# Kernel optimization log

Measured on AMD Instinct MI355X. Metric: run time of the kernel, lower is better.

## Reference

```python
import math
import jax, jax.numpy as jnp
import numpy as np

B, T, D, H, E, K = 2, 2048, 1024, 16, 8, 2
HD = D // H                      # head_dim = 64
CAP = math.ceil(1.25 * B * T / E)  # capacity per expert = 640
NEG = -1e9


def setup_inputs() -> dict:
    key = jax.random.key(0)
    ks = jax.random.split(key, 8)
    s = 0.02
    return {
        "x": jax.random.normal(ks[0], (B, T, D), jnp.float32),
        "ln1_g": jnp.ones((D,), jnp.float32),
        "ln1_b": jnp.zeros((D,), jnp.float32),
        "w_qkv": jax.random.normal(ks[1], (3 * D, D), jnp.float32) * s,
        "w_proj": jax.random.normal(ks[2], (D, D), jnp.float32) * s,
        "ln2_g": jnp.ones((D,), jnp.float32),
        "ln2_b": jnp.zeros((D,), jnp.float32),
        "w_gate": jax.random.normal(ks[3], (E, D), jnp.float32) * s,
        "w1": jax.random.normal(ks[4], (E, D, 4 * D), jnp.float32) * s,
        "b1": jnp.zeros((E, 4 * D), jnp.float32),
        "w2": jax.random.normal(ks[5], (E, 4 * D, D), jnp.float32) * s,
        "b2": jnp.zeros((E, D), jnp.float32),
    }


def _layernorm(x, g, b, eps=1e-5):
    m = x.mean(-1, keepdims=True)
    v = ((x - m) ** 2).mean(-1, keepdims=True)
    return (x - m) * jax.lax.rsqrt(v + eps) * g + b


def _rope(q, k):
    # q,k: [B,T,H,HD]; rotate-half RoPE with half_dim = HD//2 frequencies
    half = HD // 2
    pos = jnp.arange(T, dtype=jnp.float32)[:, None]
    inv_freq = 1.0 / (10000.0 ** (jnp.arange(0, HD, 2, dtype=jnp.float32) / HD))
    ang = pos * inv_freq                              # [T, half]
    sin = jnp.sin(ang)[None, :, None, :]
    cos = jnp.cos(ang)[None, :, None, :]

    def rot(t):
        t1, t2 = t[..., :half], t[..., half:]
        return jnp.concatenate([t1 * cos - t2 * sin, t1 * sin + t2 * cos], -1)

    return rot(q), rot(k)


def _attention(x, w_qkv, w_proj):
    qkv = (x @ w_qkv.T).reshape(B, T, H, 3 * HD)
    q, k, v = jnp.split(qkv, 3, axis=-1)              # each [B,T,H,HD]
    q, k = _rope(q, k)
    scores = jnp.einsum('bqhd,bkhd->bhqk', q, k) / math.sqrt(HD)
    causal = jnp.tril(jnp.ones((T, T), bool))
    scores = jnp.where(causal, scores, NEG)
    probs = jax.nn.softmax(scores, axis=-1)
    out = jnp.einsum('bhqk,bkhd->bqhd', probs, v).reshape(B, T, D)
    return out @ w_proj.T


def _sparse_moe(x2d, w_gate, w1, b1, w2, b2):
    # x2d: [N, D] flattened tokens. Eval mode: no noise, no dropout.
    N = x2d.shape[0]
    gates = jax.nn.softmax((x2d @ w_gate.T).astype(jnp.float32), axis=-1)  # [N,E]
    gate_vals, idx = jax.lax.top_k(gates, K)          # [N,K]
    gate_vals = gate_vals.astype(x2d.dtype)

    # Capacity enforcement: token order position within each expert
    mask = jnp.zeros((N, E), bool).at[jnp.arange(N)[:, None], idx].set(True)
    pos = jnp.cumsum(mask.astype(jnp.int32), axis=0) * mask - 1   # [N,E]
    keep = (pos < CAP) & mask
    slot = jnp.take_along_axis(pos, idx, axis=1)      # [N,K]
    kept = jnp.take_along_axis(keep, idx, axis=1)     # [N,K] bool

    # Dispatch: dropped tokens go to pad slot CAP (masked out at combine)
    slot_w = jnp.where(kept, slot, CAP).reshape(-1)   # [N*K]
    e_flat = idx.reshape(-1)                          # [N*K]
    xk = jnp.broadcast_to(x2d[:, None, :], (N, K, D)).reshape(-1, D)
    xk = xk * kept.reshape(-1, 1)
    buf = jnp.zeros((E, CAP + 1, D), x2d.dtype).at[e_flat, slot_w].set(xk)

    # Grouped expert MLP (GELU exact, matching nn.GELU default)
    h = jax.nn.gelu(jnp.einsum('ecd,edf->ecf', buf, w1) + b1[:, None, :],
                    approximate=False)
    out = jnp.einsum('ecf,efd->ecd', h, w2) + b2[:, None, :]

    # Combine: gather each token's expert output, weight by gate, mask drops
    y = out[e_flat, slot_w].reshape(N, K, D) * (gate_vals * kept)[..., None]
    return y.sum(axis=1)


def reference(x, ln1_g, ln1_b, w_qkv, w_proj, ln2_g, ln2_b,
              w_gate, w1, b1, w2, b2):
    h = x + _attention(_layernorm(x, ln1_g, ln1_b), w_qkv, w_proj)
    moe_in = _layernorm(h, ln2_g, ln2_b)
    moe_out = _sparse_moe(moe_in.reshape(B * T, D), w_gate, w1, b1, w2, b2)
    return h + moe_out.reshape(B, T, D)
```

## Files before the change

### kernel.cpp

```cpp
#include <hip/hip_runtime.h>
#include <hip/hip_bf16.h>

typedef __bf16 bf16;
typedef __attribute__((ext_vector_type(8))) __bf16 bf16x8;
typedef __attribute__((ext_vector_type(4))) __bf16 bf16x4;
typedef __attribute__((ext_vector_type(4))) float f32x4;
typedef __attribute__((ext_vector_type(16))) float f32x16;

#define NB 2
#define NT 2048
#define ND 1024
#define NH 16
#define HD_ 64
#define NE 8
#define NCAP 640
#define NTOK 4096
#define NDFF 4096

static __device__ __forceinline__ f32x4 mfma16(bf16x8 a, bf16x8 b, f32x4 c) {
  return __builtin_amdgcn_mfma_f32_16x16x32_bf16(a, b, c, 0, 0, 0);
}
static __device__ __forceinline__ f32x16 mfma32(bf16x8 a, bf16x8 b, f32x16 c) {
  return __builtin_amdgcn_mfma_f32_32x32x16_bf16(a, b, c, 0, 0, 0);
}
static __device__ __forceinline__ unsigned pk2(float a, float b) {
  union { __bf16 h[2]; unsigned u; } z;
  z.h[0] = (__bf16)a; z.h[1] = (__bf16)b;
  return z.u;
}
static __device__ __forceinline__ void gload_lds16(const bf16* g, bf16* l) {
  __builtin_amdgcn_global_load_lds(
      (const __attribute__((address_space(1))) unsigned int*)g,
      (__attribute__((address_space(3))) unsigned int*)l, 16, 0, 0);
}

__global__ __launch_bounds__(256) void cvt_k(const float* __restrict__ in,
                                             bf16* __restrict__ out, int n4) {
  int i = blockIdx.x * 256 + threadIdx.x;
  int stride = gridDim.x * 256;
  for (; i < n4; i += stride) {
    f32x4 v = ((const f32x4*)in)[i];
    bf16x4 o;
    o[0] = (bf16)v[0]; o[1] = (bf16)v[1]; o[2] = (bf16)v[2]; o[3] = (bf16)v[3];
    ((bf16x4*)out)[i] = o;
  }
}

__global__ __launch_bounds__(256) void transpose_k(const float* __restrict__ in,
                                                   bf16* __restrict__ out, int R, int C) {
  __shared__ float tile[64][65];
  const size_t zoff = (size_t)blockIdx.z * R * C;
  in += zoff; out += zoff;
  const int c0 = blockIdx.x * 64, r0 = blockIdx.y * 64;
  const int tx = threadIdx.x & 15, ty = threadIdx.x >> 4;
#pragma unroll
  for (int i = 0; i < 4; i++) {
    const int r = i * 16 + ty;
    f32x4 v = *(const f32x4*)(in + (size_t)(r0 + r) * C + c0 + tx * 4);
    *(f32x4*)&tile[r][tx * 4] = v;
  }
  __syncthreads();
#pragma unroll
  for (int i = 0; i < 4; i++) {
    const int rr = i * 16 + ty;
    bf16x4 o;
#pragma unroll
    for (int j = 0; j < 4; j++) o[j] = (bf16)tile[tx * 4 + j][rr];
    *(bf16x4*)(out + (size_t)(c0 + rr) * R + r0 + tx * 4) = o;
  }
}

__global__ __launch_bounds__(256) void transpose_v_k(const bf16* __restrict__ v,
                                                     bf16* __restrict__ vT) {
  __shared__ bf16 tile[32][33];
  int bh = blockIdx.z;
  const bf16* in = v + (size_t)bh * NT * HD_;
  bf16* out = vT + (size_t)bh * HD_ * NT;
  int t0 = blockIdx.x * 32, d0 = blockIdx.y * 32;
  int tx = threadIdx.x, ty = threadIdx.y;
#pragma unroll
  for (int i = 0; i < 4; i++)
    tile[ty + i * 8][tx] = in[(size_t)(t0 + ty + i * 8) * HD_ + d0 + tx];
  __syncthreads();
#pragma unroll
  for (int i = 0; i < 4; i++)
    out[(size_t)(d0 + ty + i * 8) * NT + t0 + tx] = tile[tx][ty + i * 8];
}

__global__ void rope_tab_k(float* __restrict__ tab) {
  int t = blockIdx.x, i = threadIdx.x;
  float inv = powf(10000.f, -(float)(2 * i) * (1.f / 64.f));
  float ang = (float)t * inv;
  float s, c;
  sincosf(ang, &s, &c);
  tab[(t * 32 + i) * 2] = s;
  tab[(t * 32 + i) * 2 + 1] = c;
}

template <bool BF16OUT>
__global__ __launch_bounds__(256) void ln_k(const float* __restrict__ in,
                                            const float* __restrict__ g,
                                            const float* __restrict__ bb,
                                            bf16* __restrict__ outb,
                                            float* __restrict__ outf) {
  const int row = blockIdx.x;
  const float* xr = in + (size_t)row * ND;
  const int tid = threadIdx.x, lane = tid & 63, wid = tid >> 6;
  f32x4 v = ((const f32x4*)xr)[tid];
  float s = v[0] + v[1] + v[2] + v[3];
  float sq = v[0] * v[0] + v[1] * v[1] + v[2] * v[2] + v[3] * v[3];
#pragma unroll
  for (int m = 1; m < 64; m <<= 1) {
    s += __shfl_xor(s, m, 64);
    sq += __shfl_xor(sq, m, 64);
  }
  __shared__ float red[8];
  if (lane == 0) { red[wid] = s; red[4 + wid] = sq; }
  __syncthreads();
  s = red[0] + red[1] + red[2] + red[3];
  sq = red[4] + red[5] + red[6] + red[7];
  float mean = s * (1.f / 1024.f);
  float var = sq * (1.f / 1024.f) - mean * mean;
  float rs = rsqrtf(var + 1e-5f);
#pragma unroll
  for (int c = 0; c < 4; c++) {
    int col = tid * 4 + c;
    float y = (v[c] - mean) * rs * g[col] + bb[col];
    if constexpr (BF16OUT) outb[(size_t)row * ND + col] = (bf16)y;
    else outf[(size_t)row * ND + col] = y;
  }
}

#define EPI_SPLIT_QKV 0
#define EPI_ADD_X 1
#define EPI_BIAS_GELU 2
#define EPI_STORE 3

template <int EPI, int STAGE, bool PAD>
__global__ __launch_bounds__(256) void gemm_bt_k(
    const bf16* __restrict__ A, const bf16* __restrict__ Bw,
    const int M, const int N, const int K, const int nsplit,
    const size_t zA, const size_t zB, const size_t zOut, const size_t zBias,
    const float* __restrict__ bias, const float* __restrict__ Xadd,
    void* __restrict__ Out, bf16* __restrict__ k_out, bf16* __restrict__ v_out) {
  const int z = blockIdx.z;
  const int ze = z / nsplit;
  const int kc = z - ze * nsplit;
  const int klen = K / nsplit;
  const int kb = kc * klen;
  const int nst = klen / 64;
  const int m0 = blockIdx.y * 128, n0 = blockIdx.x * 128;
  const int tid = threadIdx.x, lane = tid & 63, wid = tid >> 6;
  const int wm = (wid >> 1) * 64, wn = (wid & 1) * 64;
  const int l15 = lane & 15, ksl = lane >> 4;
  constexpr int LDB = (STAGE == 1 && PAD) ? 72 : 64;
  __shared__ __align__(16) bf16 As[128 * LDB];
  __shared__ __align__(16) bf16 Bs[128 * LDB];
  f32x4 acc[4][4];
#pragma unroll
  for (int i = 0; i < 4; i++)
#pragma unroll
    for (int j = 0; j < 4; j++) acc[i][j] = (f32x4){0.f, 0.f, 0.f, 0.f};

  if constexpr (STAGE == 0) {
    const int lr = lane >> 3, lc = (lane & 7) * 8;
    const bf16* Ag = A + zA * ze + (size_t)(m0 + wid * 32 + lr) * K + kb + lc;
    const bf16* Bg = Bw + zB * ze + (size_t)(n0 + wid * 32 + lr) * K + kb + lc;
    for (int s = 0; s < nst; ++s) {
      __syncthreads();
#pragma unroll
      for (int it = 0; it < 4; it++) {
        gload_lds16(Ag + (size_t)(it * 8) * K + s * 64, &As[(wid * 32 + it * 8) * 64]);
        gload_lds16(Bg + (size_t)(it * 8) * K + s * 64, &Bs[(wid * 32 + it * 8) * 64]);
      }
      __syncthreads();
#pragma unroll
      for (int kk = 0; kk < 2; kk++) {
        bf16x8 af[4], bfr[4];
        const int ko = kk * 32 + ksl * 8;
#pragma unroll
        for (int i = 0; i < 4; i++)
          af[i] = *(const bf16x8*)&As[(wm + i * 16 + l15) * 64 + ko];
#pragma unroll
        for (int j = 0; j < 4; j++)
          bfr[j] = *(const bf16x8*)&Bs[(wn + j * 16 + l15) * 64 + ko];
#pragma unroll
        for (int i = 0; i < 4; i++)
#pragma unroll
          for (int j = 0; j < 4; j++)
            acc[i][j] = mfma16(af[i], bfr[j], acc[i][j]);
      }
    }
  } else {
    const int sr = tid >> 3, sc = (tid & 7) * 8;
    const bf16* Ag = A + zA * ze + (size_t)(m0 + sr) * K + kb + sc;
    const bf16* Bg = Bw + zB * ze + (size_t)(n0 + sr) * K + kb + sc;
    bf16x8 av[4], bv[4];
#pragma unroll
    for (int it = 0; it < 4; it++) {
      av[it] = *(const bf16x8*)(Ag + (size_t)(it * 32) * K);
      bv[it] = *(const bf16x8*)(Bg + (size_t)(it * 32) * K);
    }
    for (int s = 0; s < nst; ++s) {
      __syncthreads();
#pragma unroll
      for (int it = 0; it < 4; it++) {
        *(bf16x8*)&As[(sr + it * 32) * LDB + sc] = av[it];
        *(bf16x8*)&Bs[(sr + it * 32) * LDB + sc] = bv[it];
      }
      __syncthreads();
      if (s + 1 < nst) {
#pragma unroll
        for (int it = 0; it < 4; it++) {
          av[it] = *(const bf16x8*)(Ag + (size_t)(it * 32) * K + (s + 1) * 64);
          bv[it] = *(const bf16x8*)(Bg + (size_t)(it * 32) * K + (s + 1) * 64);
        }
      }
#pragma unroll
      for (int kk = 0; kk < 2; kk++) {
        bf16x8 af[4], bfr[4];
        const int ko = kk * 32 + ksl * 8;
#pragma unroll
        for (int i = 0; i < 4; i++)
          af[i] = *(const bf16x8*)&As[(wm + i * 16 + l15) * LDB + ko];
#pragma unroll
        for (int j = 0; j < 4; j++)
          bfr[j] = *(const bf16x8*)&Bs[(wn + j * 16 + l15) * LDB + ko];
#pragma unroll
        for (int i = 0; i < 4; i++)
#pragma unroll
          for (int j = 0; j < 4; j++)
            acc[i][j] = mfma16(af[i], bfr[j], acc[i][j]);
      }
    }
  }

#pragma unroll
  for (int i = 0; i < 4; i++) {
#pragma unroll
    for (int j = 0; j < 4; j++) {
      const int mb = m0 + wm + i * 16 + ksl * 4;
      const int nc = n0 + wn + j * 16 + l15;
#pragma unroll
      for (int r = 0; r < 4; r++) {
        const int mr = mb + r;
        float vacc = acc[i][j][r];
        if constexpr (EPI == EPI_SPLIT_QKV) {
          const int h = nc / 192;
          const int rr = nc - h * 192;
          const int which = rr >> 6;
          const int d = rr & 63;
          const int b = mr >> 11, t = mr & 2047;
          bf16* dst = (which == 0) ? (bf16*)Out : (which == 1 ? k_out : v_out);
          dst[(((size_t)(b * NH + h)) * NT + t) * HD_ + d] = (bf16)vacc;
        } else if constexpr (EPI == EPI_ADD_X) {
          ((float*)Out)[(size_t)mr * N + nc] = vacc + Xadd[(size_t)mr * N + nc];
        } else if constexpr (EPI == EPI_BIAS_GELU) {
          float x = vacc + bias[zBias * ze + nc];
          float u2 = x * (2.3020882f + 0.10294772f * x * x);
          float gl = x / (1.f + exp2f(-u2));
          ((bf16*)Out)[zOut * ze + (size_t)mr * N + nc] = (bf16)gl;
        } else {
          ((bf16*)Out)[((size_t)kc * NE + ze) * zOut + (size_t)mr * N + nc] = (bf16)vacc;
        }
      }
    }
  }
}

__global__ __launch_bounds__(256) void rope_k(bf16* __restrict__ q, bf16* __restrict__ k,
                                              const float* __restrict__ tab) {
  const int bh = blockIdx.y;
  const int t = blockIdx.x * 4 + (threadIdx.x >> 6);
  const int d = threadIdx.x & 63;
  const size_t row = ((size_t)bh * NT + t) * HD_;
  const int i = d & 31;
  const float sn = tab[(t * 32 + i) * 2], cs = tab[(t * 32 + i) * 2 + 1];
  {
    float a = (float)q[row + d];
    float b2 = (float)q[row + (d ^ 32)];
    float o = (d < 32) ? (a * cs - b2 * sn) : (b2 * sn + a * cs);
    q[row + d] = (bf16)(o * 0.18033688011112042f);
  }
  {
    float a = (float)k[row + d];
    float b2 = (float)k[row + (d ^ 32)];
    float o = (d < 32) ? (a * cs - b2 * sn) : (b2 * sn + a * cs);
    k[row + d] = (bf16)o;
  }
}

__global__ __launch_bounds__(256) void attn_k(const bf16* __restrict__ q,
                                              const bf16* __restrict__ k,
                                              const bf16* __restrict__ vT,
                                              bf16* __restrict__ attn_out) {
  __shared__ __align__(16) bf16 Kt[64 * 64];
  __shared__ __align__(16) bf16 Vt[64 * 64];
  const int bid = blockIdx.x;
  const int bh = bid & 31;
  const int ti = (bid >> 5) & 7;
  const int qt = (bid >> 8) ? (15 - ti) : ti;
  const int q0 = qt * 128;
  const int tid = threadIdx.x, lane = tid & 63, wid = tid >> 6;
  const int l31 = lane & 31, hi = lane >> 5;
  const int q0w = q0 + wid * 32;
  const int qrow = q0w + l31;
  const size_t base = (size_t)bh * (NT * HD_);
  const size_t baseT = (size_t)bh * (HD_ * NT);

  bf16x8 qf[4];
#pragma unroll
  for (int ks = 0; ks < 4; ks++)
    qf[ks] = *(const bf16x8*)(q + base + (size_t)qrow * HD_ + ks * 16 + hi * 8);

  f32x16 ot0, ot1;
#pragma unroll
  for (int r = 0; r < 16; r++) { ot0[r] = 0.f; ot1[r] = 0.f; }
  float m2 = -1e30f, l = 0.f;

  const int ntiles = qt * 2 + 2;
  const int swz = (l31 & 7);
  const int strow = tid >> 3, stc = tid & 7;
  const int cw0 = ((stc ^ (strow & 7)) * 8);
  bf16x8 kr[2], vr[2];
#pragma unroll
  for (int rr = 0; rr < 2; rr++) {
    kr[rr] = *(const bf16x8*)(k + base + (size_t)(strow + rr * 32) * HD_ + stc * 8);
    vr[rr] = *(const bf16x8*)(vT + baseT + (size_t)(strow + rr * 32) * NT + stc * 8);
  }

  for (int t = 0; t < ntiles; t++) {
    const int kv0 = t * 64;
    __syncthreads();
#pragma unroll
    for (int rr = 0; rr < 2; rr++) {
      *(bf16x8*)&Kt[(strow + rr * 32) * 64 + cw0] = kr[rr];
      *(bf16x8*)&Vt[(strow + rr * 32) * 64 + cw0] = vr[rr];
    }
    __syncthreads();
    if (t + 1 < ntiles) {
      const int kn = kv0 + 64;
#pragma unroll
      for (int rr = 0; rr < 2; rr++) {
        kr[rr] = *(const bf16x8*)(k + base + (size_t)(kn + strow + rr * 32) * HD_ + stc * 8);
        vr[rr] = *(const bf16x8*)(vT + baseT + (size_t)(strow + rr * 32) * NT + kn + stc * 8);
      }
    }
    if (kv0 > q0w + 31) continue;

    f32x16 s0, s1;
#pragma unroll
    for (int r = 0; r < 16; r++) { s0[r] = 0.f; s1[r] = 0.f; }
#pragma unroll
    for (int ks = 0; ks < 4; ks++) {
      const int cw = (((ks * 2 + hi) ^ swz) * 8);
      bf16x8 ka0 = *(const bf16x8*)&Kt[l31 * 64 + cw];
      bf16x8 ka1 = *(const bf16x8*)&Kt[(l31 + 32) * 64 + cw];
      s0 = mfma32(ka0, qf[ks], s0);
      s1 = mfma32(ka1, qf[ks], s1);
    }

    float p[32];
#pragma unroll
    for (int r = 0; r < 16; r++) { p[r] = s0[r]; p[16 + r] = s1[r]; }
    if (kv0 + 63 > q0w) {
#pragma unroll
      for (int sub = 0; sub < 2; sub++)
#pragma unroll
        for (int r = 0; r < 16; r++) {
          int kvg = kv0 + sub * 32 + (r & 3) + 8 * (r >> 2) + 4 * hi;
          if (kvg > qrow) p[sub * 16 + r] = -1e30f;
        }
    }
    float tm = p[0];
#pragma unroll
    for (int r = 1; r < 32; r++) tm = fmaxf(tm, p[r]);
    tm = fmaxf(tm, __shfl_xor(tm, 32, 64));
    if (!__all(tm <= m2 + 8.f)) {
      float mn = fmaxf(m2, tm);
      float sf = exp2f(m2 - mn);
      m2 = mn;
      l *= sf;
#pragma unroll
      for (int r = 0; r < 16; r++) { ot0[r] *= sf; ot1[r] *= sf; }
    }
    float ts = 0.f;
#pragma unroll
    for (int r = 0; r < 32; r++) { p[r] = exp2f(p[r] - m2); ts += p[r]; }
    ts += __shfl_xor(ts, 32, 64);
    l += ts;

#pragma unroll
    for (int ks = 0; ks < 4; ks++) {
      const int i0 = (ks >> 1) * 16 + (ks & 1) * 8;
      unsigned Aw = pk2(p[i0 + 0], p[i0 + 1]);
      unsigned Bw = pk2(p[i0 + 2], p[i0 + 3]);
      unsigned Cw = pk2(p[i0 + 4], p[i0 + 5]);
      unsigned Dw = pk2(p[i0 + 6], p[i0 + 7]);
      unsigned xA = (unsigned)__shfl_xor((int)Aw, 32, 64);
      unsigned xB = (unsigned)__shfl_xor((int)Bw, 32, 64);
      unsigned xC = (unsigned)__shfl_xor((int)Cw, 32, 64);
      unsigned xD = (unsigned)__shfl_xor((int)Dw, 32, 64);
      union { unsigned u[4]; bf16x8 v; } pa;
      pa.u[0] = hi ? xC : Aw;
      pa.u[1] = hi ? xD : Bw;
      pa.u[2] = hi ? Cw : xA;
      pa.u[3] = hi ? Dw : xB;
      const int cw = (((ks * 2 + hi) ^ swz) * 8);
      bf16x8 va0 = *(const bf16x8*)&Vt[l31 * 64 + cw];
      bf16x8 va1 = *(const bf16x8*)&Vt[(l31 + 32) * 64 + cw];
      ot0 = mfma32(va0, pa.v, ot0);
      ot1 = mfma32(va1, pa.v, ot1);
    }
  }

  const int b = bh >> 4, h = bh & 15;
  const float inv = 1.f / l;
  const size_t orow = ((size_t)(b * NT + qrow)) * ND + h * 64;
#pragma unroll
  for (int g = 0; g < 4; g++) {
    bf16x4 w0, w1;
#pragma unroll
    for (int c = 0; c < 4; c++) {
      w0[c] = (bf16)(ot0[g * 4 + c] * inv);
      w1[c] = (bf16)(ot1[g * 4 + c] * inv);
    }
    *(bf16x4*)(attn_out + orow + g * 8 + 4 * hi) = w0;
    *(bf16x4*)(attn_out + orow + 32 + g * 8 + 4 * hi) = w1;
  }
}

__global__ __launch_bounds__(256) void gate_k(const float* __restrict__ moe_in,
                                              const float* __restrict__ w_gate,
                                              int* __restrict__ idx, float* __restrict__ gv) {
  __shared__ float wg[8 * 1024];
  for (int i = threadIdx.x; i < 8192; i += 256) wg[i] = w_gate[i];
  __syncthreads();
  const int lane = threadIdx.x & 63, wid = threadIdx.x >> 6;
  for (int tt = 0; tt < 4; tt++) {
    const int n = blockIdx.x * 16 + wid * 4 + tt;
    const float* xr = moe_in + (size_t)n * ND;
    float a[8];
#pragma unroll
    for (int e = 0; e < 8; e++) a[e] = 0.f;
    for (int d0 = lane * 4; d0 < 1024; d0 += 256) {
      f32x4 xv = *(const f32x4*)(xr + d0);
#pragma unroll
      for (int e = 0; e < 8; e++) {
        const float* wr = &wg[e * 1024 + d0];
        a[e] += xv[0] * wr[0] + xv[1] * wr[1] + xv[2] * wr[2] + xv[3] * wr[3];
      }
    }
#pragma unroll
    for (int e = 0; e < 8; e++)
#pragma unroll
      for (int m = 1; m < 64; m <<= 1) a[e] += __shfl_xor(a[e], m, 64);
    if (lane == 0) {
      float mx = a[0];
#pragma unroll
      for (int e = 1; e < 8; e++) mx = fmaxf(mx, a[e]);
      float p[8], se = 0.f;
#pragma unroll
      for (int e = 0; e < 8; e++) { p[e] = expf(a[e] - mx); se += p[e]; }
      float inv = 1.f / se;
#pragma unroll
      for (int e = 0; e < 8; e++) p[e] *= inv;
      int i1 = 0; float v1 = p[0];
#pragma unroll
      for (int e = 1; e < 8; e++) if (p[e] > v1) { v1 = p[e]; i1 = e; }
      int i2 = -1; float v2 = -1.f;
#pragma unroll
      for (int e = 0; e < 8; e++) if (e != i1 && p[e] > v2) { v2 = p[e]; i2 = e; }
      idx[n * 2] = i1; idx[n * 2 + 1] = i2;
      gv[n * 2] = v1; gv[n * 2 + 1] = v2;
    }
  }
}

__global__ void scan_k(const int* __restrict__ idx, int* __restrict__ slot,
                       int* __restrict__ kept) {
  const int lane = threadIdx.x;
  int base[8];
#pragma unroll
  for (int e = 0; e < 8; e++) base[e] = 0;
  const unsigned long long lm = (lane == 63) ? ~0ull : ((1ull << (lane + 1)) - 1);
  for (int c = 0; c < 64; c++) {
    const int n = c * 64 + lane;
    const int e0 = idx[n * 2], e1 = idx[n * 2 + 1];
    int s0 = 0, s1 = 0;
#pragma unroll
    for (int e = 0; e < 8; e++) {
      unsigned long long m0 = __ballot(e0 == e);
      unsigned long long m1 = __ballot(e1 == e);
      unsigned long long m = m0 | m1;
      int pref = __popcll(m & lm);
      if (e0 == e) s0 = base[e] + pref - 1;
      if (e1 == e) s1 = base[e] + pref - 1;
      base[e] += __popcll(m);
    }
    slot[n * 2] = s0; slot[n * 2 + 1] = s1;
    kept[n * 2] = (s0 < NCAP) ? 1 : 0;
    kept[n * 2 + 1] = (s1 < NCAP) ? 1 : 0;
  }
}

__global__ __launch_bounds__(64) void scatter_k(const float* __restrict__ moe_in,
                                                const int* __restrict__ idx,
                                                const int* __restrict__ slot,
                                                const int* __restrict__ kept,
                                                bf16* __restrict__ buf) {
  const int a = blockIdx.x;
  if (!kept[a]) return;
  const int n = a >> 1;
  const int e = idx[a], s = slot[a];
  const float* src = moe_in + (size_t)n * ND;
  bf16* dst = buf + ((size_t)e * NCAP + s) * ND;
  for (int c = threadIdx.x * 4; c < 1024; c += 256) {
    f32x4 v = *(const f32x4*)(src + c);
    bf16x4 o;
    o[0] = (bf16)v[0]; o[1] = (bf16)v[1]; o[2] = (bf16)v[2]; o[3] = (bf16)v[3];
    *(bf16x4*)(dst + c) = o;
  }
}

__global__ __launch_bounds__(256) void gather_k(const float* __restrict__ h,
                                                const bf16* __restrict__ eout,
                                                const int* __restrict__ idx,
                                                const int* __restrict__ slot,
                                                const int* __restrict__ kept,
                                                const float* __restrict__ gv,
                                                const float* __restrict__ b2,
                                                float* __restrict__ out) {
  const size_t PS = (size_t)NE * NCAP * ND;
  const int n = blockIdx.x;
  const int k0 = kept[n * 2], k1 = kept[n * 2 + 1];
  const int i0 = idx[n * 2], i1 = idx[n * 2 + 1];
  const float g0 = k0 ? gv[n * 2] : 0.f;
  const float g1 = k1 ? gv[n * 2 + 1] : 0.f;
  const size_t r0 = k0 ? ((size_t)i0 * NCAP + slot[n * 2]) * ND : 0;
  const size_t r1 = k1 ? ((size_t)i1 * NCAP + slot[n * 2 + 1]) * ND : 0;
  const int c = threadIdx.x * 4;
  f32x4 o = *(const f32x4*)(h + (size_t)n * ND + c);
  if (k0) {
    bf16x4 ea = *(const bf16x4*)(eout + r0 + c);
    bf16x4 eb = *(const bf16x4*)(eout + PS + r0 + c);
    f32x4 bb = *(const f32x4*)(b2 + i0 * ND + c);
#pragma unroll
    for (int cc = 0; cc < 4; cc++)
      o[cc] += g0 * ((float)ea[cc] + (float)eb[cc] + bb[cc]);
  }
  if (k1) {
    bf16x4 ea = *(const bf16x4*)(eout + r1 + c);
    bf16x4 eb = *(const bf16x4*)(eout + PS + r1 + c);
    f32x4 bb = *(const f32x4*)(b2 + i1 * ND + c);
#pragma unroll
    for (int cc = 0; cc < 4; cc++)
      o[cc] += g1 * ((float)ea[cc] + (float)eb[cc] + bb[cc]);
  }
  *(f32x4*)(out + (size_t)n * ND + c) = o;
}

extern "C" void kernel_launch(void* const* d_in, const int* in_sizes, int n_in,
                              void* d_out, int out_size, void* d_ws, size_t ws_size,
                              hipStream_t stream) {
  (void)in_sizes; (void)n_in; (void)out_size;
  const float* x      = (const float*)d_in[0];
  const float* ln1_g  = (const float*)d_in[1];
  const float* ln1_b  = (const float*)d_in[2];
  const float* w_qkv  = (const float*)d_in[3];
  const float* w_proj = (const float*)d_in[4];
  const float* ln2_g  = (const float*)d_in[5];
  const float* ln2_b  = (const float*)d_in[6];
  const float* w_gate = (const float*)d_in[7];
  const float* w1     = (const float*)d_in[8];
  const float* b1     = (const float*)d_in[9];
  const float* w2     = (const float*)d_in[10];
  const float* b2     = (const float*)d_in[11];
  float* out = (float*)d_out;

  char* ws = (char*)d_ws;
  size_t off = 0;
  auto alloc = [&](size_t bytes) -> char* {
    char* p = ws + off;
    off += (bytes + 255) & ~(size_t)255;
    return p;
  };
  bf16* w1t    = (bf16*)alloc((size_t)NE * NDFF * ND * 2);
  bf16* w2t    = (bf16*)alloc((size_t)NE * ND * NDFF * 2);
  bf16* wqkvb  = (bf16*)alloc((size_t)3 * ND * ND * 2);
  bf16* wprojb = (bf16*)alloc((size_t)ND * ND * 2);
  float* hbufr = (float*)alloc((size_t)NTOK * ND * 4);
  float* moein = (float*)alloc((size_t)NTOK * ND * 4);
  float* ropet = (float*)alloc((size_t)NT * 32 * 2 * 4);
  int*   idx   = (int*)alloc((size_t)NTOK * 2 * 4);
  int*   slot  = (int*)alloc((size_t)NTOK * 2 * 4);
  int*   kept  = (int*)alloc((size_t)NTOK * 2 * 4);
  float* gv    = (float*)alloc((size_t)NTOK * 2 * 4);
  char*  S     = alloc((size_t)62914560);
  if (off > ws_size) return;

  const size_t MB8 = (size_t)8388608;
  bf16* xn    = (bf16*)(S);
  bf16* qp    = (bf16*)(S + MB8);
  bf16* kp    = (bf16*)(S + 2 * MB8);
  bf16* vp    = (bf16*)(S + 3 * MB8);
  bf16* attnp = (bf16*)(S + 4 * MB8);
  bf16* vTp   = (bf16*)(S);
  bf16* hbuf  = (bf16*)(S);
  bf16* buf   = (bf16*)(S + (size_t)41943040);
  bf16* eout  = (bf16*)(S + (size_t)41943040);

  dim3 tb(32, 8);
  cvt_k<<<2048, 256, 0, stream>>>(w_qkv, wqkvb, 3 * ND * ND / 4);
  cvt_k<<<1024, 256, 0, stream>>>(w_proj, wprojb, ND * ND / 4);
  transpose_k<<<dim3(NDFF / 64, ND / 64, NE), 256, 0, stream>>>(w1, w1t, ND, NDFF);
  transpose_k<<<dim3(ND / 64, NDFF / 64, NE), 256, 0, stream>>>(w2, w2t, NDFF, ND);
  rope_tab_k<<<NT, 32, 0, stream>>>(ropet);
  ln_k<true><<<NTOK, 256, 0, stream>>>(x, ln1_g, ln1_b, xn, nullptr);
  gemm_bt_k<EPI_SPLIT_QKV, 0, false><<<dim3(3 * ND / 128, NTOK / 128, 1), 256, 0, stream>>>(
      xn, wqkvb, NTOK, 3 * ND, ND, 1, 0, 0, 0, 0, nullptr, nullptr, qp, kp, vp);
  transpose_v_k<<<dim3(NT / 32, HD_ / 32, NB * NH), tb, 0, stream>>>(vp, vTp);
  rope_k<<<dim3(NT / 4, NB * NH), 256, 0, stream>>>(qp, kp, ropet);
  attn_k<<<512, 256, 0, stream>>>(qp, kp, vTp, attnp);
  gemm_bt_k<EPI_ADD_X, 1, true><<<dim3(ND / 128, NTOK / 128, 1), 256, 0, stream>>>(
      attnp, wprojb, NTOK, ND, ND, 1, 0, 0, 0, 0, nullptr, x, hbufr, nullptr, nullptr);
  ln_k<false><<<NTOK, 256, 0, stream>>>(hbufr, ln2_g, ln2_b, nullptr, moein);
  gate_k<<<NTOK / 16, 256, 0, stream>>>(moein, w_gate, idx, gv);
  scan_k<<<1, 64, 0, stream>>>(idx, slot, kept);
  scatter_k<<<NTOK * 2, 64, 0, stream>>>(moein, idx, slot, kept, buf);
  gemm_bt_k<EPI_BIAS_GELU, 0, false><<<dim3(NDFF / 128, NCAP / 128, NE), 256, 0, stream>>>(
      buf, w1t, NCAP, NDFF, ND, 1, (size_t)NCAP * ND, (size_t)NDFF * ND,
      (size_t)NCAP * NDFF, NDFF, b1, nullptr, hbuf, nullptr, nullptr);
  gemm_bt_k<EPI_STORE, 1, true><<<dim3(ND / 128, NCAP / 128, NE * 2), 256, 0, stream>>>(
      hbuf, w2t, NCAP, ND, NDFF, 2, (size_t)NCAP * NDFF, (size_t)ND * NDFF,
      (size_t)NCAP * ND, 0, nullptr, nullptr, eout, nullptr, nullptr);
  gather_k<<<NTOK, 256, 0, stream>>>(hbufr, eout, idx, slot, kept, gv, b2, out);
}
```

Before: 459.9 us.

## Fuse fp32 expert-weight transpose and bf16 conversion into MoE GEMM loads

Drops the separate transpose_k passes over w1 and w2 and adds a GEMM variant that reads the fp32 expert weights directly in their row-major K-by-N layout. It converts them to bf16 and writes them transposed into a swizzled LDS tile. This removes a full read and write of both large weight tensors plus two launches. In exchange, the GEMM now reads twice the bytes per weight tile (fp32 instead of bf16), does scalar LDS stores, and uses a fast reciprocal in the GELU.

```diff
diff --git a/kernel.cpp b/kernel.cpp
--- a/kernel.cpp
+++ b/kernel.cpp
@@ -43,30 +43,6 @@
     bf16x4 o;
     o[0] = (bf16)v[0]; o[1] = (bf16)v[1]; o[2] = (bf16)v[2]; o[3] = (bf16)v[3];
     ((bf16x4*)out)[i] = o;
-  }
-}
-
-__global__ __launch_bounds__(256) void transpose_k(const float* __restrict__ in,
-                                                   bf16* __restrict__ out, int R, int C) {
-  __shared__ float tile[64][65];
-  const size_t zoff = (size_t)blockIdx.z * R * C;
-  in += zoff; out += zoff;
-  const int c0 = blockIdx.x * 64, r0 = blockIdx.y * 64;
-  const int tx = threadIdx.x & 15, ty = threadIdx.x >> 4;
-#pragma unroll
-  for (int i = 0; i < 4; i++) {
-    const int r = i * 16 + ty;
-    f32x4 v = *(const f32x4*)(in + (size_t)(r0 + r) * C + c0 + tx * 4);
-    *(f32x4*)&tile[r][tx * 4] = v;
-  }
-  __syncthreads();
-#pragma unroll
-  for (int i = 0; i < 4; i++) {
-    const int rr = i * 16 + ty;
-    bf16x4 o;
-#pragma unroll
-    for (int j = 0; j < 4; j++) o[j] = (bf16)tile[tx * 4 + j][rr];
-    *(bf16x4*)(out + (size_t)(c0 + rr) * R + r0 + tx * 4) = o;
   }
 }
 
@@ -133,27 +109,19 @@
 
 #define EPI_SPLIT_QKV 0
 #define EPI_ADD_X 1
-#define EPI_BIAS_GELU 2
-#define EPI_STORE 3
-
-template <int EPI, int STAGE, bool PAD>
+
+template <int EPI, int STAGE>
 __global__ __launch_bounds__(256) void gemm_bt_k(
     const bf16* __restrict__ A, const bf16* __restrict__ Bw,
-    const int M, const int N, const int K, const int nsplit,
-    const size_t zA, const size_t zB, const size_t zOut, const size_t zBias,
-    const float* __restrict__ bias, const float* __restrict__ Xadd,
-    void* __restrict__ Out, bf16* __restrict__ k_out, bf16* __restrict__ v_out) {
-  const int z = blockIdx.z;
-  const int ze = z / nsplit;
-  const int kc = z - ze * nsplit;
-  const int klen = K / nsplit;
-  const int kb = kc * klen;
-  const int nst = klen / 64;
+    const int M, const int N, const int K,
+    const float* __restrict__ Xadd, void* __restrict__ Out,
+    bf16* __restrict__ k_out, bf16* __restrict__ v_out) {
   const int m0 = blockIdx.y * 128, n0 = blockIdx.x * 128;
   const int tid = threadIdx.x, lane = tid & 63, wid = tid >> 6;
   const int wm = (wid >> 1) * 64, wn = (wid & 1) * 64;
   const int l15 = lane & 15, ksl = lane >> 4;
-  constexpr int LDB = (STAGE == 1 && PAD) ? 72 : 64;
+  const int nst = K / 64;
+  constexpr int LDB = (STAGE == 1) ? 72 : 64;
   __shared__ __align__(16) bf16 As[128 * LDB];
   __shared__ __align__(16) bf16 Bs[128 * LDB];
   f32x4 acc[4][4];
@@ -164,8 +132,8 @@
 
   if constexpr (STAGE == 0) {
     const int lr = lane >> 3, lc = (lane & 7) * 8;
-    const bf16* Ag = A + zA * ze + (size_t)(m0 + wid * 32 + lr) * K + kb + lc;
-    const bf16* Bg = Bw + zB * ze + (size_t)(n0 + wid * 32 + lr) * K + kb + lc;
+    const bf16* Ag = A + (size_t)(m0 + wid * 32 + lr) * K + lc;
+    const bf16* Bg = Bw + (size_t)(n0 + wid * 32 + lr) * K + lc;
     for (int s = 0; s < nst; ++s) {
       __syncthreads();
 #pragma unroll
@@ -193,8 +161,8 @@
     }
   } else {
     const int sr = tid >> 3, sc = (tid & 7) * 8;
-    const bf16* Ag = A + zA * ze + (size_t)(m0 + sr) * K + kb + sc;
-    const bf16* Bg = Bw + zB * ze + (size_t)(n0 + sr) * K + kb + sc;
+    const bf16* Ag = A + (size_t)(m0 + sr) * K + sc;
+    const bf16* Bg = Bw + (size_t)(n0 + sr) * K + sc;
     bf16x8 av[4], bv[4];
 #pragma unroll
     for (int it = 0; it < 4; it++) {
@@ -253,15 +221,112 @@
           const int b = mr >> 11, t = mr & 2047;
           bf16* dst = (which == 0) ? (bf16*)Out : (which == 1 ? k_out : v_out);
           dst[(((size_t)(b * NH + h)) * NT + t) * HD_ + d] = (bf16)vacc;
-        } else if constexpr (EPI == EPI_ADD_X) {
+        } else {
           ((float*)Out)[(size_t)mr * N + nc] = vacc + Xadd[(size_t)mr * N + nc];
-        } else if constexpr (EPI == EPI_BIAS_GELU) {
+        }
+      }
+    }
+  }
+}
+
+#define EPI_BIAS_GELU 0
+#define EPI_STORE 1
+
+template <int EPI>
+__global__ __launch_bounds__(256) void gemm_bf32_k(
+    const bf16* __restrict__ A, const float* __restrict__ Bw,
+    const int M, const int N, const int K, const int nsplit,
+    const size_t zA, const size_t zB, const size_t zOut, const size_t zBias,
+    const float* __restrict__ bias, bf16* __restrict__ Out) {
+  const int z = blockIdx.z;
+  const int ze = z / nsplit;
+  const int kc = z - ze * nsplit;
+  const int klen = K / nsplit;
+  const int kb = kc * klen;
+  const int nst = klen / 64;
+  const int m0 = blockIdx.y * 128, n0 = blockIdx.x * 128;
+  const int tid = threadIdx.x, lane = tid & 63, wid = tid >> 6;
+  const int wm = (wid >> 1) * 64, wn = (wid & 1) * 64;
+  const int l15 = lane & 15, ksl = lane >> 4;
+  __shared__ __align__(16) bf16 As[128 * 72];
+  __shared__ __align__(16) bf16 Bs[128 * 72];
+  f32x4 acc[4][4];
+#pragma unroll
+  for (int i = 0; i < 4; i++)
+#pragma unroll
+    for (int j = 0; j < 4; j++) acc[i][j] = (f32x4){0.f, 0.f, 0.f, 0.f};
+
+  const int sr = tid >> 3, sc = (tid & 7) * 8;
+  const bf16* Ag = A + zA * ze + (size_t)(m0 + sr) * K + kb + sc;
+  const int kt = tid >> 2, ng = tid & 3;
+  const float* Bg = Bw + zB * ze + (size_t)(kb + kt) * N + n0 + ng * 32;
+
+  bf16x8 av[4];
+  f32x4 bv[8];
+#pragma unroll
+  for (int it = 0; it < 4; it++) av[it] = *(const bf16x8*)(Ag + (size_t)(it * 32) * K);
+#pragma unroll
+  for (int it = 0; it < 8; it++) bv[it] = *(const f32x4*)(Bg + it * 4);
+
+  for (int s = 0; s < nst; ++s) {
+    __syncthreads();
+#pragma unroll
+    for (int it = 0; it < 4; it++)
+      *(bf16x8*)&As[(sr + it * 32) * 72 + sc] = av[it];
+#pragma unroll
+    for (int it = 0; it < 8; it++) {
+#pragma unroll
+      for (int j = 0; j < 4; j++) {
+        const int n = ng * 32 + it * 4 + j;
+        Bs[n * 72 + (kt ^ ((n >> 5) << 4))] = (bf16)bv[it][j];
+      }
+    }
+    __syncthreads();
+    if (s + 1 < nst) {
+#pragma unroll
+      for (int it = 0; it < 4; it++)
+        av[it] = *(const bf16x8*)(Ag + (size_t)(it * 32) * K + (s + 1) * 64);
+#pragma unroll
+      for (int it = 0; it < 8; it++)
+        bv[it] = *(const f32x4*)(Bg + (size_t)((s + 1) * 64) * N + it * 4);
+    }
+#pragma unroll
+    for (int kk = 0; kk < 2; kk++) {
+      bf16x8 af[4], bfr[4];
+      const int ko = kk * 32 + ksl * 8;
+#pragma unroll
+      for (int i = 0; i < 4; i++)
+        af[i] = *(const bf16x8*)&As[(wm + i * 16 + l15) * 72 + ko];
+#pragma unroll
+      for (int j = 0; j < 4; j++) {
+        const int col = wn + j * 16 + l15;
+        bfr[j] = *(const bf16x8*)&Bs[col * 72 + (ko ^ ((col >> 5) << 4))];
+      }
+#pragma unroll
+      for (int i = 0; i < 4; i++)
+#pragma unroll
+        for (int j = 0; j < 4; j++)
+          acc[i][j] = mfma16(af[i], bfr[j], acc[i][j]);
+    }
+  }
+
+#pragma unroll
+  for (int i = 0; i < 4; i++) {
+#pragma unroll
+    for (int j = 0; j < 4; j++) {
+      const int mb = m0 + wm + i * 16 + ksl * 4;
+      const int nc = n0 + wn + j * 16 + l15;
+#pragma unroll
+      for (int r = 0; r < 4; r++) {
+        const int mr = mb + r;
+        float vacc = acc[i][j][r];
+        if constexpr (EPI == EPI_BIAS_GELU) {
           float x = vacc + bias[zBias * ze + nc];
           float u2 = x * (2.3020882f + 0.10294772f * x * x);
-          float gl = x / (1.f + exp2f(-u2));
-          ((bf16*)Out)[zOut * ze + (size_t)mr * N + nc] = (bf16)gl;
+          float gl = x * __builtin_amdgcn_rcpf(1.f + exp2f(-u2));
+          Out[zOut * ze + (size_t)mr * N + nc] = (bf16)gl;
         } else {
-          ((bf16*)Out)[((size_t)kc * NE + ze) * zOut + (size_t)mr * N + nc] = (bf16)vacc;
+          Out[((size_t)kc * NE + ze) * zOut + (size_t)mr * N + nc] = (bf16)vacc;
         }
       }
     }
@@ -585,8 +650,6 @@
     off += (bytes + 255) & ~(size_t)255;
     return p;
   };
-  bf16* w1t    = (bf16*)alloc((size_t)NE * NDFF * ND * 2);
-  bf16* w2t    = (bf16*)alloc((size_t)NE * ND * NDFF * 2);
   bf16* wqkvb  = (bf16*)alloc((size_t)3 * ND * ND * 2);
   bf16* wprojb = (bf16*)alloc((size_t)ND * ND * 2);
   float* hbufr = (float*)alloc((size_t)NTOK * ND * 4);
@@ -613,26 +676,24 @@
   dim3 tb(32, 8);
   cvt_k<<<2048, 256, 0, stream>>>(w_qkv, wqkvb, 3 * ND * ND / 4);
   cvt_k<<<1024, 256, 0, stream>>>(w_proj, wprojb, ND * ND / 4);
-  transpose_k<<<dim3(NDFF / 64, ND / 64, NE), 256, 0, stream>>>(w1, w1t, ND, NDFF);
-  transpose_k<<<dim3(ND / 64, NDFF / 64, NE), 256, 0, stream>>>(w2, w2t, NDFF, ND);
   rope_tab_k<<<NT, 32, 0, stream>>>(ropet);
   ln_k<true><<<NTOK, 256, 0, stream>>>(x, ln1_g, ln1_b, xn, nullptr);
-  gemm_bt_k<EPI_SPLIT_QKV, 0, false><<<dim3(3 * ND / 128, NTOK / 128, 1), 256, 0, stream>>>(
-      xn, wqkvb, NTOK, 3 * ND, ND, 1, 0, 0, 0, 0, nullptr, nullptr, qp, kp, vp);
+  gemm_bt_k<EPI_SPLIT_QKV, 0><<<dim3(3 * ND / 128, NTOK / 128, 1), 256, 0, stream>>>(
+      xn, wqkvb, NTOK, 3 * ND, ND, nullptr, qp, kp, vp);
   transpose_v_k<<<dim3(NT / 32, HD_ / 32, NB * NH), tb, 0, stream>>>(vp, vTp);
   rope_k<<<dim3(NT / 4, NB * NH), 256, 0, stream>>>(qp, kp, ropet);
   attn_k<<<512, 256, 0, stream>>>(qp, kp, vTp, attnp);
-  gemm_bt_k<EPI_ADD_X, 1, true><<<dim3(ND / 128, NTOK / 128, 1), 256, 0, stream>>>(
-      attnp, wprojb, NTOK, ND, ND, 1, 0, 0, 0, 0, nullptr, x, hbufr, nullptr, nullptr);
+  gemm_bt_k<EPI_ADD_X, 1><<<dim3(ND / 128, NTOK / 128, 1), 256, 0, stream>>>(
+      attnp, wprojb, NTOK, ND, ND, x, hbufr, nullptr, nullptr);
   ln_k<false><<<NTOK, 256, 0, stream>>>(hbufr, ln2_g, ln2_b, nullptr, moein);
   gate_k<<<NTOK / 16, 256, 0, stream>>>(moein, w_gate, idx, gv);
   scan_k<<<1, 64, 0, stream>>>(idx, slot, kept);
   scatter_k<<<NTOK * 2, 64, 0, stream>>>(moein, idx, slot, kept, buf);
-  gemm_bt_k<EPI_BIAS_GELU, 0, false><<<dim3(NDFF / 128, NCAP / 128, NE), 256, 0, stream>>>(
-      buf, w1t, NCAP, NDFF, ND, 1, (size_t)NCAP * ND, (size_t)NDFF * ND,
-      (size_t)NCAP * NDFF, NDFF, b1, nullptr, hbuf, nullptr, nullptr);
-  gemm_bt_k<EPI_STORE, 1, true><<<dim3(ND / 128, NCAP / 128, NE * 2), 256, 0, stream>>>(
-      hbuf, w2t, NCAP, ND, NDFF, 2, (size_t)NCAP * NDFF, (size_t)ND * NDFF,
-      (size_t)NCAP * ND, 0, nullptr, nullptr, eout, nullptr, nullptr);
+  gemm_bf32_k<EPI_BIAS_GELU><<<dim3(NDFF / 128, NCAP / 128, NE), 256, 0, stream>>>(
+      buf, w1, NCAP, NDFF, ND, 1, (size_t)NCAP * ND, (size_t)ND * NDFF,
+      (size_t)NCAP * NDFF, NDFF, b1, hbuf);
+  gemm_bf32_k<EPI_STORE><<<dim3(ND / 128, NCAP / 128, NE * 2), 256, 0, stream>>>(
+      hbuf, w2, NCAP, ND, NDFF, 2, (size_t)NCAP * NDFF, (size_t)NDFF * ND,
+      (size_t)NCAP * ND, 0, nullptr, eout);
   gather_k<<<NTOK, 256, 0, stream>>>(hbufr, eout, idx, slot, kept, gv, b2, out);
 }
```

After: 483.3 us. 1.05x slower.
